# Kernel tuning notes

Hardware: AMD Instinct MI355X
Metric: run time of the kernel (lower is better)

The kernel has to match this reference:

```python
import jax, jax.numpy as jnp
import numpy as np

SIZE1 = 4096
SIZE2 = 4096
EMB = 32
T = 4
B = 8192
K = 20          # self.k
TAU = 1.0       # self.tau
HID = 64        # hidden_dim


def setup_inputs() -> dict:
    key = jax.random.key(0)
    ks = jax.random.split(key, 12)
    return {
        "time": jax.random.randint(ks[0], (B,), 0, T),
        "index1": jax.random.randint(ks[1], (B,), 0, SIZE1),
        "index2": jax.random.randint(ks[2], (B,), 0, SIZE2),
        "residuals": jax.random.normal(ks[3], (T, SIZE1, SIZE2), jnp.float32),
        "means": jax.random.normal(ks[4], (T, SIZE1, SIZE2), jnp.float32),
        "stds": jax.random.uniform(ks[5], (T, SIZE1, SIZE2), jnp.float32),
        "emb1": jax.random.normal(ks[6], (SIZE1, EMB), jnp.float32) * 0.1,
        "emb2": jax.random.normal(ks[7], (SIZE2, EMB), jnp.float32) * 0.1,
        "W1": jax.random.normal(ks[8], (HID, 8), jnp.float32) * 0.1,
        "b1": jnp.zeros((HID,), jnp.float32),
        "Wm": jax.random.normal(ks[9], (1, HID), jnp.float32) * 0.1,
        "bm": jnp.zeros((1,), jnp.float32),
        "Ws": jax.random.normal(ks[10], (1, HID), jnp.float32) * 0.1,
        "bs": jnp.zeros((1,), jnp.float32),
    }


def _knn_feats(y_ctx, idx, emb):
    """One branch of compute_feats. y_ctx: [B,N], idx: [B] int, emb: [N,d]."""
    q = emb[idx]                                             # [B, d]
    # torch.cdist p=2 via (||a||^2 + ||b||^2 - 2ab^T)^(1/2)
    d2 = (q * q).sum(1, keepdims=True) + (emb * emb).sum(1)[None, :] - 2.0 * (q @ emb.T)
    sim = jnp.sqrt(jnp.maximum(d2, 0.0)) + 0.001             # [B, N]
    rows = jnp.arange(idx.shape[0])
    sim = sim.at[rows, idx].set(0.0)                         # zero self-similarity
    w = jnp.exp(-sim / TAU)
    # argsort ascending, take the K largest excluding the very largest (self)
    nbr = jnp.argsort(w, axis=1)[:, -(K + 1):-1]             # [B, K]
    sel = jnp.take_along_axis(y_ctx, nbr, axis=1)            # [B, K]
    wsel = jnp.take_along_axis(w, nbr, axis=1)               # [B, K]
    wsum = wsel.sum(1, keepdims=True)
    return jnp.concatenate([
        (sel * wsel).sum(1, keepdims=True) / wsum,           # weighted mean
        wsum,                                                # weight mass
        jnp.std(sel, axis=1, keepdims=True, ddof=1),         # torch.std (unbiased)
    ], axis=1)                                               # [B, 3]


def reference(time, index1, index2, residuals, means, stds,
              emb1, emb2, W1, b1, Wm, bm, Ws, bs):
    mean = means[time, index1, index2]                       # [B]
    std = stds[time, index1, index2]                         # [B]
    y2_context = residuals[time, index1, :]                  # [B, SIZE2]
    y1_context = residuals[time, :, index2]                  # [B, SIZE1]
    f1 = _knn_feats(y1_context, index1, emb1)                # [B, 3]
    f2 = _knn_feats(y2_context, index2, emb2)                # [B, 3]
    feats = jnp.concatenate([f1, f2, mean[:, None], std[:, None]], axis=1)  # [B, 8]
    h = jnp.maximum(feats @ W1.T + b1, 0.0)                  # clamp(min=0)
    mean_outlier = (h @ Wm.T + bm)[:, 0]
    std_outlier = (h @ Ws.T + bs)[:, 0]
    return mean_outlier, std_outlier
```

## Files before the change

### kernel.cpp

```cpp
#include <hip/hip_runtime.h>
#include <math.h>

#define SZ1 4096
#define SZ2 4096
#define EMBD 32
#define KNN 20
#define HID 64

__global__ __launch_bounds__(256) void knn_kernel(
    const float* __restrict__ emb1, const float* __restrict__ emb2,
    int* __restrict__ nbr, float* __restrict__ wv)
{
    const int bid    = blockIdx.x;
    const int branch = bid >> 12;
    const int i      = bid & 4095;
    const float* emb = branch ? emb2 : emb1;
    const int tid    = threadIdx.x;

    __shared__ float  sim[4096];
    __shared__ float4 qs[8];
    __shared__ float  red_v[4];
    __shared__ int    red_i[4];

    if (tid < 8) qs[tid] = ((const float4*)(emb + (size_t)i * EMBD))[tid];
    __syncthreads();

    float4 q[8];
    float qq = 0.f;
#pragma unroll
    for (int d = 0; d < 8; ++d) {
        q[d] = qs[d];
        qq += q[d].x * q[d].x + q[d].y * q[d].y + q[d].z * q[d].z + q[d].w * q[d].w;
    }

    for (int j = tid; j < 4096; j += 256) {
        const float4* row = (const float4*)(emb + (size_t)j * EMBD);
        float dot = 0.f, ee = 0.f;
#pragma unroll
        for (int d = 0; d < 8; ++d) {
            float4 e = row[d];
            dot += e.x * q[d].x + e.y * q[d].y + e.z * q[d].z + e.w * q[d].w;
            ee  += e.x * e.x + e.y * e.y + e.z * e.z + e.w * e.w;
        }
        float d2 = qq + ee - 2.f * dot;
        float s  = sqrtf(fmaxf(d2, 0.f)) + 0.001f;
        sim[j] = (j == i) ? 1e30f : s;
    }
    __syncthreads();

    int*   nb_out = nbr + ((size_t)branch * SZ1 + i) * KNN;
    float* w_out  = wv  + ((size_t)branch * SZ1 + i) * KNN;

    for (int k = 0; k < KNN; ++k) {
        float best = 1e30f; int bi = -1;
        for (int j = tid; j < 4096; j += 256) {
            float v = sim[j];
            if (v < best) { best = v; bi = j; }
        }
#pragma unroll
        for (int off = 32; off; off >>= 1) {
            float ov = __shfl_down(best, off, 64);
            int   oi = __shfl_down(bi, off, 64);
            if (ov < best) { best = ov; bi = oi; }
        }
        if ((tid & 63) == 0) { red_v[tid >> 6] = best; red_i[tid >> 6] = bi; }
        __syncthreads();
        if (tid == 0) {
            float bv = red_v[0]; int bj = red_i[0];
#pragma unroll
            for (int w2 = 1; w2 < 4; ++w2)
                if (red_v[w2] < bv) { bv = red_v[w2]; bj = red_i[w2]; }
            nb_out[k] = bj;
            w_out[k]  = expf(-bv);
            sim[bj]   = 1e30f;
        }
        __syncthreads();
    }
}

__global__ __launch_bounds__(256) void feat_mlp_kernel(
    const int* __restrict__ time, const int* __restrict__ idx1,
    const int* __restrict__ idx2,
    const float* __restrict__ residuals, const float* __restrict__ means,
    const float* __restrict__ stds,
    const int* __restrict__ nbr, const float* __restrict__ wv,
    const float* __restrict__ W1, const float* __restrict__ b1,
    const float* __restrict__ Wm, const float* __restrict__ bm,
    const float* __restrict__ Ws, const float* __restrict__ bs,
    float* __restrict__ out, int B)
{
    const int wave = threadIdx.x >> 6;
    const int lane = threadIdx.x & 63;
    const int s    = blockIdx.x * 4 + wave;
    if (s >= B) return;

    const int t  = time[s];
    const int i1 = idx1[s];
    const int i2 = idx2[s];
    const size_t base = (size_t)t * SZ1 * SZ2;

    const int half = lane >> 5;
    const int k    = lane & 31;

    float y = 0.f, w = 0.f;
    if (k < KNN) {
        if (half == 0) {
            const size_t o = ((size_t)0 * SZ1 + i1) * KNN + k;
            const int nb = nbr[o];
            y = residuals[base + (size_t)nb * SZ2 + i2];
            w = wv[o];
        } else {
            const size_t o = ((size_t)1 * SZ1 + i2) * KNN + k;
            const int nb = nbr[o];
            y = residuals[base + (size_t)i1 * SZ2 + nb];
            w = wv[o];
        }
    }

    float wy = w * y, sw = w, sy = y;
#pragma unroll
    for (int off = 16; off; off >>= 1) {
        wy += __shfl_xor(wy, off, 32);
        sw += __shfl_xor(sw, off, 32);
        sy += __shfl_xor(sy, off, 32);
    }
    const float m   = sy * (1.f / KNN);
    float dev = (k < KNN) ? (y - m) : 0.f;
    float ss  = dev * dev;
#pragma unroll
    for (int off = 16; off; off >>= 1) ss += __shfl_xor(ss, off, 32);

    const float wmean = wy / sw;
    const float sd    = sqrtf(ss * (1.f / (KNN - 1)));

    const float f_wm1 = __shfl(wmean, 0, 64);
    const float f_sw1 = __shfl(sw,    0, 64);
    const float f_sd1 = __shfl(sd,    0, 64);
    const float f_wm2 = __shfl(wmean, 32, 64);
    const float f_sw2 = __shfl(sw,    32, 64);
    const float f_sd2 = __shfl(sd,    32, 64);

    const float mn  = means[base + (size_t)i1 * SZ2 + i2];
    const float sdv = stds [base + (size_t)i1 * SZ2 + i2];

    const float feats[8] = { f_wm1, f_sw1, f_sd1, f_wm2, f_sw2, f_sd2, mn, sdv };

    const float* wrow = W1 + lane * 8;
    float h = b1[lane];
#pragma unroll
    for (int f = 0; f < 8; ++f) h += feats[f] * wrow[f];
    h = fmaxf(h, 0.f);

    float mo = h * Wm[lane];
    float so = h * Ws[lane];
#pragma unroll
    for (int off = 32; off; off >>= 1) {
        mo += __shfl_xor(mo, off, 64);
        so += __shfl_xor(so, off, 64);
    }
    if (lane == 0) {
        out[s]     = mo + bm[0];
        out[B + s] = so + bs[0];
    }
}

extern "C" void kernel_launch(void* const* d_in, const int* in_sizes, int n_in,
                              void* d_out, int out_size, void* d_ws, size_t ws_size,
                              hipStream_t stream)
{
    const int*   time      = (const int*)d_in[0];
    const int*   idx1      = (const int*)d_in[1];
    const int*   idx2      = (const int*)d_in[2];
    const float* residuals = (const float*)d_in[3];
    const float* means     = (const float*)d_in[4];
    const float* stds      = (const float*)d_in[5];
    const float* emb1      = (const float*)d_in[6];
    const float* emb2      = (const float*)d_in[7];
    const float* W1        = (const float*)d_in[8];
    const float* b1        = (const float*)d_in[9];
    const float* Wm        = (const float*)d_in[10];
    const float* bm        = (const float*)d_in[11];
    const float* Ws        = (const float*)d_in[12];
    const float* bs        = (const float*)d_in[13];
    float* out = (float*)d_out;

    const int B = in_sizes[0];

    int*   nbr = (int*)d_ws;
    float* wv  = (float*)((char*)d_ws + (size_t)2 * SZ1 * KNN * sizeof(int));

    knn_kernel<<<2 * SZ1, 256, 0, stream>>>(emb1, emb2, nbr, wv);
    feat_mlp_kernel<<<(B + 3) / 4, 256, 0, stream>>>(
        time, idx1, idx2, residuals, means, stds, nbr, wv,
        W1, b1, Wm, bm, Ws, bs, out, B);
}
```

Baseline: 1.046 ms.

## Replace iterative argmin top-k with histogram radix select over register-held distances

Replaces the 20-round block-wide argmin over a shared 4096-entry similarity array with a multi-level 256-bin histogram select. Distances stay in registers, candidates below the threshold bin are compacted into shared memory, and a single wave does the final top-20 on up to 192 candidates. Each block now handles two query rows so every embedding load is shared between them, and row norms are precomputed in a separate kernel. This removes about 40 block barriers per row and the redundant norm work, at the cost of extra kernels, shared-memory atomics and more complex tie handling near the threshold.

```diff
diff --git a/kernel.cpp b/kernel.cpp
--- a/kernel.cpp
+++ b/kernel.cpp
@@ -6,76 +6,207 @@
 #define EMBD 32
 #define KNN 20
 #define HID 64
-
-__global__ __launch_bounds__(256) void knn_kernel(
+#define SELCAP 192
+
+__global__ __launch_bounds__(256) void norms_kernel(
     const float* __restrict__ emb1, const float* __restrict__ emb2,
+    float* __restrict__ norms)
+{
+    const int j = blockIdx.x * 256 + threadIdx.x;
+    const float* emb = (j < SZ1) ? emb1 : emb2;
+    const int r = j & (SZ1 - 1);
+    const float4* row = (const float4*)(emb + (size_t)r * EMBD);
+    float ee = 0.f;
+#pragma unroll
+    for (int d = 0; d < 8; ++d) {
+        float4 e = row[d];
+        ee += e.x * e.x + e.y * e.y + e.z * e.z + e.w * e.w;
+    }
+    norms[j] = ee;
+}
+
+struct SelShared {
+    unsigned int hist[256];
+    float        cand_d2[SELCAP];
+    int          cand_i[SELCAP];
+    float        red_mn[4], red_mx[4];
+    unsigned int wsum[4];
+    unsigned int bc_b, bc_cumb, bc_prev, ncand;
+};
+
+__device__ __forceinline__ void select20(
+    float (&d2c)[16], int qidx, SelShared& sh,
+    int tid, int lane, int wid,
+    int* __restrict__ nb_out, float* __restrict__ w_out)
+{
+    unsigned int alive = 0xFFFFu;
+    if (tid == (qidx & 255)) alive &= ~(1u << (qidx >> 8));
+    unsigned int cand = 0u;
+
+    float mn = 1e30f, mx = -1e30f;
+#pragma unroll
+    for (int r = 0; r < 16; ++r)
+        if (alive & (1u << r)) { mn = fminf(mn, d2c[r]); mx = fmaxf(mx, d2c[r]); }
+#pragma unroll
+    for (int off = 32; off; off >>= 1) {
+        mn = fminf(mn, __shfl_xor(mn, off, 64));
+        mx = fmaxf(mx, __shfl_xor(mx, off, 64));
+    }
+    if (lane == 0) { sh.red_mn[wid] = mn; sh.red_mx[wid] = mx; }
+    __syncthreads();
+    mn = fminf(fminf(sh.red_mn[0], sh.red_mn[1]), fminf(sh.red_mn[2], sh.red_mn[3]));
+    mx = fmaxf(fmaxf(sh.red_mx[0], sh.red_mx[1]), fmaxf(sh.red_mx[2], sh.red_mx[3]));
+
+    float lo = mn;
+    float binw = (mx - mn) * (1.f / 256.f);
+    unsigned int base = 0;
+    bool done = false;
+
+    for (int lvl = 0; lvl < 6 && !done; ++lvl) {
+        const float scale = (binw > 0.f) ? (1.f / binw) : 0.f;
+        sh.hist[tid] = 0;
+        __syncthreads();
+#pragma unroll
+        for (int r = 0; r < 16; ++r)
+            if (alive & (1u << r)) {
+                float bf = fminf(fmaxf((d2c[r] - lo) * scale, 0.f), 255.f);
+                atomicAdd(&sh.hist[(int)bf], 1u);
+            }
+        __syncthreads();
+
+        unsigned int h = sh.hist[tid];
+        unsigned int c = h;
+#pragma unroll
+        for (int off = 1; off < 64; off <<= 1) {
+            unsigned int n = __shfl_up(c, off, 64);
+            if (lane >= off) c += n;
+        }
+        if (lane == 63) sh.wsum[wid] = c;
+        __syncthreads();
+        if (wid > 0) c += sh.wsum[0];
+        if (wid > 1) c += sh.wsum[1];
+        if (wid > 2) c += sh.wsum[2];
+        const unsigned int ct = base + c;
+        if (ct >= KNN && (ct - h) < KNN) {
+            sh.bc_b = (unsigned int)tid; sh.bc_cumb = ct; sh.bc_prev = ct - h;
+        }
+        __syncthreads();
+        const int b = (int)sh.bc_b;
+        const unsigned int cumb = sh.bc_cumb;
+        const unsigned int prevc = sh.bc_prev;
+
+#pragma unroll
+        for (int r = 0; r < 16; ++r)
+            if (alive & (1u << r)) {
+                float bf = fminf(fmaxf((d2c[r] - lo) * scale, 0.f), 255.f);
+                int bin = (int)bf;
+                if (bin < b)      { cand |= (1u << r); alive &= ~(1u << r); }
+                else if (bin > b) { alive &= ~(1u << r); }
+            }
+
+        if (cumb <= SELCAP) { cand |= alive; done = true; }
+        else {
+            base = prevc;
+            lo = lo + (float)b * binw;
+            binw *= (1.f / 256.f);
+            if (binw < 1e-37f) { cand |= alive; done = true; }
+        }
+        __syncthreads();
+    }
+    if (!done) cand |= alive;
+
+    __syncthreads();
+    if (tid == 0) sh.ncand = 0;
+    __syncthreads();
+#pragma unroll
+    for (int r = 0; r < 16; ++r)
+        if (cand & (1u << r)) {
+            unsigned int slot = atomicAdd(&sh.ncand, 1u);
+            if (slot < SELCAP) {
+                sh.cand_d2[slot] = d2c[r];
+                sh.cand_i[slot]  = (r << 8) + tid;
+            }
+        }
+    __syncthreads();
+
+    if (wid == 0) {
+        int cnt = (int)sh.ncand; if (cnt > SELCAP) cnt = SELCAP;
+        float va = (lane < cnt)        ? sh.cand_d2[lane]       : 1e30f;
+        float vb = (lane + 64 < cnt)   ? sh.cand_d2[lane + 64]  : 1e30f;
+        float vc = (lane + 128 < cnt)  ? sh.cand_d2[lane + 128] : 1e30f;
+        float kd2 = 0.f; int ks = 0;
+#pragma unroll
+        for (int k = 0; k < KNN; ++k) {
+            float bv = va; int bs = lane;
+            if (vb < bv) { bv = vb; bs = lane + 64; }
+            if (vc < bv) { bv = vc; bs = lane + 128; }
+#pragma unroll
+            for (int off = 32; off; off >>= 1) {
+                float ov = __shfl_xor(bv, off, 64);
+                int   os = __shfl_xor(bs, off, 64);
+                if (ov < bv || (ov == bv && os < bs)) { bv = ov; bs = os; }
+            }
+            if (lane == (bs & 63)) {
+                if (bs < 64) va = 1e30f; else if (bs < 128) vb = 1e30f; else vc = 1e30f;
+            }
+            if (lane == k) { kd2 = bv; ks = bs; }
+        }
+        if (lane < KNN) {
+            nb_out[lane] = sh.cand_i[ks];
+            w_out[lane]  = expf(-(sqrtf(kd2) + 0.001f));
+        }
+    }
+}
+
+__global__ __launch_bounds__(256) void knn2_kernel(
+    const float* __restrict__ emb1, const float* __restrict__ emb2,
+    const float* __restrict__ norms,
     int* __restrict__ nbr, float* __restrict__ wv)
 {
-    const int bid    = blockIdx.x;
-    const int branch = bid >> 12;
-    const int i      = bid & 4095;
+    const int g0     = blockIdx.x * 2;
+    const int branch = g0 >> 12;
+    const int i0     = g0 & 4095;
+    const int i1     = i0 + 1;
     const float* emb = branch ? emb2 : emb1;
-    const int tid    = threadIdx.x;
-
-    __shared__ float  sim[4096];
-    __shared__ float4 qs[8];
-    __shared__ float  red_v[4];
-    __shared__ int    red_i[4];
-
-    if (tid < 8) qs[tid] = ((const float4*)(emb + (size_t)i * EMBD))[tid];
-    __syncthreads();
-
-    float4 q[8];
-    float qq = 0.f;
-#pragma unroll
-    for (int d = 0; d < 8; ++d) {
-        q[d] = qs[d];
-        qq += q[d].x * q[d].x + q[d].y * q[d].y + q[d].z * q[d].z + q[d].w * q[d].w;
-    }
-
-    for (int j = tid; j < 4096; j += 256) {
+    const float* nrm = norms + branch * SZ1;
+    const int tid  = threadIdx.x;
+    const int lane = tid & 63;
+    const int wid  = tid >> 6;
+
+    __shared__ float4 qs[16];
+    __shared__ SelShared sh;
+
+    if (tid < 16)
+        qs[tid] = ((const float4*)(emb + (size_t)(i0 + (tid >> 3)) * EMBD))[tid & 7];
+    __syncthreads();
+
+    float4 q0[8], q1[8];
+#pragma unroll
+    for (int d = 0; d < 8; ++d) { q0[d] = qs[d]; q1[d] = qs[8 + d]; }
+    const float qq0 = nrm[i0];
+    const float qq1 = nrm[i1];
+
+    float d2c0[16], d2c1[16];
+#pragma unroll
+    for (int r = 0; r < 16; ++r) {
+        const int j = (r << 8) + tid;
         const float4* row = (const float4*)(emb + (size_t)j * EMBD);
-        float dot = 0.f, ee = 0.f;
+        float dot0 = 0.f, dot1 = 0.f;
 #pragma unroll
         for (int d = 0; d < 8; ++d) {
             float4 e = row[d];
-            dot += e.x * q[d].x + e.y * q[d].y + e.z * q[d].z + e.w * q[d].w;
-            ee  += e.x * e.x + e.y * e.y + e.z * e.z + e.w * e.w;
-        }
-        float d2 = qq + ee - 2.f * dot;
-        float s  = sqrtf(fmaxf(d2, 0.f)) + 0.001f;
-        sim[j] = (j == i) ? 1e30f : s;
-    }
-    __syncthreads();
-
-    int*   nb_out = nbr + ((size_t)branch * SZ1 + i) * KNN;
-    float* w_out  = wv  + ((size_t)branch * SZ1 + i) * KNN;
-
-    for (int k = 0; k < KNN; ++k) {
-        float best = 1e30f; int bi = -1;
-        for (int j = tid; j < 4096; j += 256) {
-            float v = sim[j];
-            if (v < best) { best = v; bi = j; }
-        }
-#pragma unroll
-        for (int off = 32; off; off >>= 1) {
-            float ov = __shfl_down(best, off, 64);
-            int   oi = __shfl_down(bi, off, 64);
-            if (ov < best) { best = ov; bi = oi; }
-        }
-        if ((tid & 63) == 0) { red_v[tid >> 6] = best; red_i[tid >> 6] = bi; }
-        __syncthreads();
-        if (tid == 0) {
-            float bv = red_v[0]; int bj = red_i[0];
-#pragma unroll
-            for (int w2 = 1; w2 < 4; ++w2)
-                if (red_v[w2] < bv) { bv = red_v[w2]; bj = red_i[w2]; }
-            nb_out[k] = bj;
-            w_out[k]  = expf(-bv);
-            sim[bj]   = 1e30f;
-        }
-        __syncthreads();
-    }
+            dot0 += e.x * q0[d].x + e.y * q0[d].y + e.z * q0[d].z + e.w * q0[d].w;
+            dot1 += e.x * q1[d].x + e.y * q1[d].y + e.z * q1[d].z + e.w * q1[d].w;
+        }
+        const float ee = nrm[j];
+        d2c0[r] = fmaxf(qq0 + ee - 2.f * dot0, 0.f);
+        d2c1[r] = fmaxf(qq1 + ee - 2.f * dot1, 0.f);
+    }
+
+    int*   nb0 = nbr + ((size_t)branch * SZ1 + i0) * KNN;
+    float* w0  = wv  + ((size_t)branch * SZ1 + i0) * KNN;
+    select20(d2c0, i0, sh, tid, lane, wid, nb0, w0);
+    select20(d2c1, i1, sh, tid, lane, wid, nb0 + KNN, w0 + KNN);
 }
 
 __global__ __launch_bounds__(256) void feat_mlp_kernel(
@@ -186,10 +317,13 @@
 
     const int B = in_sizes[0];
 
-    int*   nbr = (int*)d_ws;
-    float* wv  = (float*)((char*)d_ws + (size_t)2 * SZ1 * KNN * sizeof(int));
-
-    knn_kernel<<<2 * SZ1, 256, 0, stream>>>(emb1, emb2, nbr, wv);
+    const size_t NBR_BYTES = (size_t)2 * SZ1 * KNN * sizeof(int);
+    int*   nbr   = (int*)d_ws;
+    float* wv    = (float*)((char*)d_ws + NBR_BYTES);
+    float* norms = (float*)((char*)d_ws + 2 * NBR_BYTES);
+
+    norms_kernel<<<(2 * SZ1) / 256, 256, 0, stream>>>(emb1, emb2, norms);
+    knn2_kernel<<<SZ1, 256, 0, stream>>>(emb1, emb2, norms, nbr, wv);
     feat_mlp_kernel<<<(B + 3) / 4, 256, 0, stream>>>(
         time, idx1, idx2, residuals, means, stds, nbr, wv,
         W1, b1, Wm, bm, Ws, bs, out, B);
```

New measurement: 1.455 ms. 39.1% more time.

## Replace iterative top-K argmin with histogram radix select and single-wave final sort

Applied to the files above, without the earlier changes.

Swaps the 20 rounds of block-wide argmin, each with two barriers, for a multi-level 256-bin histogram selection over squared distances. It narrows down to a small candidate set of at most 192 entries, which one wave then sorts with shuffle-based argmin. sqrt and exp are deferred to the selected K only, and launch bounds request higher occupancy. The cost is extra shared-memory atomics and histogram passes, with subtle tie and overflow handling when many values fall in one bin.

```diff
diff --git a/kernel.cpp b/kernel.cpp
--- a/kernel.cpp
+++ b/kernel.cpp
@@ -6,8 +6,9 @@
 #define EMBD 32
 #define KNN 20
 #define HID 64
-
-__global__ __launch_bounds__(256) void knn_kernel(
+#define SELCAP 192
+
+__global__ __launch_bounds__(256, 4) void knn_kernel(
     const float* __restrict__ emb1, const float* __restrict__ emb2,
     int* __restrict__ nbr, float* __restrict__ wv)
 {
@@ -15,12 +16,18 @@
     const int branch = bid >> 12;
     const int i      = bid & 4095;
     const float* emb = branch ? emb2 : emb1;
-    const int tid    = threadIdx.x;
-
-    __shared__ float  sim[4096];
-    __shared__ float4 qs[8];
-    __shared__ float  red_v[4];
-    __shared__ int    red_i[4];
+    const int tid  = threadIdx.x;
+    const int lane = tid & 63;
+    const int wid  = tid >> 6;
+
+    __shared__ float        sim[4096];
+    __shared__ float4       qs[8];
+    __shared__ unsigned int hist[256];
+    __shared__ float        cand_d2[SELCAP];
+    __shared__ int          cand_i[SELCAP];
+    __shared__ float        red_mn[4], red_mx[4];
+    __shared__ unsigned int wsum[4];
+    __shared__ unsigned int bc_b, bc_cumb, bc_prev, ncand;
 
     if (tid < 8) qs[tid] = ((const float4*)(emb + (size_t)i * EMBD))[tid];
     __syncthreads();
@@ -33,7 +40,10 @@
         qq += q[d].x * q[d].x + q[d].y * q[d].y + q[d].z * q[d].z + q[d].w * q[d].w;
     }
 
-    for (int j = tid; j < 4096; j += 256) {
+    float mn = 1e30f, mx = -1e30f;
+#pragma unroll 1
+    for (int r = 0; r < 16; ++r) {
+        const int j = (r << 8) + tid;
         const float4* row = (const float4*)(emb + (size_t)j * EMBD);
         float dot = 0.f, ee = 0.f;
 #pragma unroll
@@ -42,39 +52,119 @@
             dot += e.x * q[d].x + e.y * q[d].y + e.z * q[d].z + e.w * q[d].w;
             ee  += e.x * e.x + e.y * e.y + e.z * e.z + e.w * e.w;
         }
-        float d2 = qq + ee - 2.f * dot;
-        float s  = sqrtf(fmaxf(d2, 0.f)) + 0.001f;
-        sim[j] = (j == i) ? 1e30f : s;
-    }
-    __syncthreads();
-
-    int*   nb_out = nbr + ((size_t)branch * SZ1 + i) * KNN;
-    float* w_out  = wv  + ((size_t)branch * SZ1 + i) * KNN;
-
-    for (int k = 0; k < KNN; ++k) {
-        float best = 1e30f; int bi = -1;
-        for (int j = tid; j < 4096; j += 256) {
-            float v = sim[j];
-            if (v < best) { best = v; bi = j; }
-        }
-#pragma unroll
-        for (int off = 32; off; off >>= 1) {
-            float ov = __shfl_down(best, off, 64);
-            int   oi = __shfl_down(bi, off, 64);
-            if (ov < best) { best = ov; bi = oi; }
-        }
-        if ((tid & 63) == 0) { red_v[tid >> 6] = best; red_i[tid >> 6] = bi; }
-        __syncthreads();
-        if (tid == 0) {
-            float bv = red_v[0]; int bj = red_i[0];
-#pragma unroll
-            for (int w2 = 1; w2 < 4; ++w2)
-                if (red_v[w2] < bv) { bv = red_v[w2]; bj = red_i[w2]; }
-            nb_out[k] = bj;
-            w_out[k]  = expf(-bv);
-            sim[bj]   = 1e30f;
-        }
-        __syncthreads();
+        float d2 = fmaxf(qq + ee - 2.f * dot, 0.f);
+        if (j == i) d2 = 1e30f;
+        else { mn = fminf(mn, d2); mx = fmaxf(mx, d2); }
+        sim[j] = d2;
+    }
+
+#pragma unroll
+    for (int off = 32; off; off >>= 1) {
+        mn = fminf(mn, __shfl_xor(mn, off, 64));
+        mx = fmaxf(mx, __shfl_xor(mx, off, 64));
+    }
+    if (lane == 0) { red_mn[wid] = mn; red_mx[wid] = mx; }
+    __syncthreads();
+    mn = fminf(fminf(red_mn[0], red_mn[1]), fminf(red_mn[2], red_mn[3]));
+    mx = fmaxf(fmaxf(red_mx[0], red_mx[1]), fmaxf(red_mx[2], red_mx[3]));
+
+    float lo = mn;
+    float binw = (mx - mn) * (1.f / 256.f);
+    float hi = mn + binw * 256.f;
+    unsigned int base = 0;
+    int done = 0;
+
+    for (int lvl = 0; lvl < 6; ++lvl) {
+        if (binw <= 0.f) break;
+        const float scale = 1.f / binw;
+        hist[tid] = 0;
+        if (tid == 0) bc_b = 0xFFFFFFFFu;
+        __syncthreads();
+        for (int r = 0; r < 16; ++r) {
+            const float v = sim[(r << 8) + tid];
+            if (v >= lo && v < hi) {
+                int b = (int)fminf((v - lo) * scale, 255.f);
+                atomicAdd(&hist[b], 1u);
+            }
+        }
+        __syncthreads();
+        const unsigned int h = hist[tid];
+        unsigned int c = h;
+#pragma unroll
+        for (int off = 1; off < 64; off <<= 1) {
+            unsigned int n = __shfl_up(c, off, 64);
+            if (lane >= off) c += n;
+        }
+        if (lane == 63) wsum[wid] = c;
+        __syncthreads();
+        if (wid > 0) c += wsum[0];
+        if (wid > 1) c += wsum[1];
+        if (wid > 2) c += wsum[2];
+        const unsigned int ct = base + c;
+        if (ct >= KNN && (ct - h) < KNN) {
+            bc_b = (unsigned int)tid; bc_cumb = ct; bc_prev = ct - h;
+        }
+        __syncthreads();
+        if (bc_b == 0xFFFFFFFFu) break;
+        if (bc_cumb <= SELCAP) { done = 1; break; }
+        base = bc_prev;
+        lo   = lo + (float)bc_b * binw;
+        hi   = lo + binw;
+        binw *= (1.f / 256.f);
+        __syncthreads();
+    }
+
+    const int   b_fin     = (done == 1) ? (int)bc_b : 256;
+    const float scale_fin = (binw > 0.f) ? (1.f / binw) : 0.f;
+
+    __syncthreads();
+    if (tid == 0) ncand = 0;
+    __syncthreads();
+
+    for (int r = 0; r < 16; ++r) {
+        const int j = (r << 8) + tid;
+        const float v = sim[j];
+        bool take;
+        if (done == 1)
+            take = (v < lo) ||
+                   (v < hi && (int)fminf((v - lo) * scale_fin, 255.f) <= b_fin);
+        else
+            take = (v <= hi);
+        if (take) {
+            unsigned int slot = atomicAdd(&ncand, 1u);
+            if (slot < SELCAP) { cand_d2[slot] = v; cand_i[slot] = j; }
+        }
+    }
+    __syncthreads();
+
+    if (wid == 0) {
+        int cnt = (int)ncand; if (cnt > SELCAP) cnt = SELCAP;
+        float va = (lane < cnt)       ? cand_d2[lane]       : 1e30f;
+        float vb = (lane + 64 < cnt)  ? cand_d2[lane + 64]  : 1e30f;
+        float vc = (lane + 128 < cnt) ? cand_d2[lane + 128] : 1e30f;
+        int*   nb_out = nbr + ((size_t)branch * SZ1 + i) * KNN;
+        float* w_out  = wv  + ((size_t)branch * SZ1 + i) * KNN;
+        float kd2 = 0.f; int ks = 0;
+#pragma unroll 1
+        for (int k = 0; k < KNN; ++k) {
+            float bv = va; int bs = lane;
+            if (vb < bv) { bv = vb; bs = lane + 64; }
+            if (vc < bv) { bv = vc; bs = lane + 128; }
+#pragma unroll
+            for (int off = 32; off; off >>= 1) {
+                float ov = __shfl_xor(bv, off, 64);
+                int   os = __shfl_xor(bs, off, 64);
+                if (ov < bv || (ov == bv && os < bs)) { bv = ov; bs = os; }
+            }
+            if (lane == (bs & 63)) {
+                if (bs < 64) va = 1e30f; else if (bs < 128) vb = 1e30f; else vc = 1e30f;
+            }
+            if (lane == k) { kd2 = bv; ks = bs; }
+        }
+        if (lane < KNN) {
+            nb_out[lane] = cand_i[ks];
+            w_out[lane]  = expf(-(sqrtf(kd2) + 0.001f));
+        }
     }
 }
 
@@ -186,8 +276,9 @@
 
     const int B = in_sizes[0];
 
+    const size_t NBR_BYTES = (size_t)2 * SZ1 * KNN * sizeof(int);
     int*   nbr = (int*)d_ws;
-    float* wv  = (float*)((char*)d_ws + (size_t)2 * SZ1 * KNN * sizeof(int));
+    float* wv  = (float*)((char*)d_ws + NBR_BYTES);
 
     knn_kernel<<<2 * SZ1, 256, 0, stream>>>(emb1, emb2, nbr, wv);
     feat_mlp_kernel<<<(B + 3) / 4, 256, 0, stream>>>(
```

Measured after the change: 0.9995 ms. 4.4% less time.
